# Kernel tuning notes

Hardware: AMD Instinct MI355X
Metric: run time of the kernel (lower is better)

The kernel has to match this reference:

```python
import jax, jax.numpy as jnp
import numpy as np

B, D_IN, NQ, D_OUT = 65536, 1024, 64, 1024
PI = float(np.pi)


def setup_inputs() -> dict:
    key = jax.random.key(0)
    ks = jax.random.split(key, 6)
    return {
        "x": jax.random.normal(ks[0], (B, D_IN), dtype=jnp.float32),
        "W_in": jax.random.normal(ks[1], (NQ, D_IN), dtype=jnp.float32) * 0.02,
        "b_in": jax.random.normal(ks[2], (NQ,), dtype=jnp.float32) * 0.02,
        "quantum_params": jax.random.normal(ks[3], (NQ, 3), dtype=jnp.float32) * 0.1,
        "W_out": jax.random.normal(ks[4], (D_OUT, NQ), dtype=jnp.float32) * 0.02,
        "b_out": jax.random.normal(ks[5], (D_OUT,), dtype=jnp.float32) * 0.02,
    }


def reference(x, W_in, b_in, quantum_params, W_out, b_out):
    # input linear + tanh: [B, NQ]
    h = jnp.tanh(x @ W_in.T + b_in)
    # quantum forward, vectorized over (batch, qubit):
    # state = cos(h*pi/2)*cos(p0) + sin(p1)*cos(p2)
    angles = h * PI
    p0, p1, p2 = quantum_params[:, 0], quantum_params[:, 1], quantum_params[:, 2]
    state = jnp.cos(angles * 0.5) * jnp.cos(p0) + jnp.sin(p1) * jnp.cos(p2)
    # output linear: [B, D_OUT]
    return state @ W_out.T + b_out
```

## Files before the change

kernel.cpp:

```cpp
#include <hip/hip_runtime.h>
#include <hip/hip_bf16.h>
#include <math.h>

#define NB 65536
#define DIN 1024
#define NQ 64
#define DOUT 1024

typedef __attribute__((ext_vector_type(8))) short bf16x8;
typedef __attribute__((ext_vector_type(4))) float f32x4;
typedef unsigned short u16;

__device__ __forceinline__ u16 f2bf(float f) {
    union { float f; unsigned u; } v; v.f = f;
    return (u16)((v.u + 0x7fffu + ((v.u >> 16) & 1u)) >> 16);
}

__device__ __forceinline__ void gll16(const void* g, void* l) {
    __builtin_amdgcn_global_load_lds(
        (const __attribute__((address_space(1))) unsigned int*)g,
        (__attribute__((address_space(3))) unsigned int*)l, 16, 0, 0);
}
__device__ __forceinline__ void gll4(const void* g, void* l) {
    __builtin_amdgcn_global_load_lds(
        (const __attribute__((address_space(1))) unsigned int*)g,
        (__attribute__((address_space(3))) unsigned int*)l, 4, 0, 0);
}

__global__ __launch_bounds__(256) void kP(const float* __restrict__ W_in,
                                          const float* __restrict__ W_out,
                                          const float* __restrict__ qp,
                                          u16* __restrict__ Wbf,
                                          u16* __restrict__ Wobf,
                                          float* __restrict__ cp0,
                                          float* __restrict__ cq) {
    int tid = blockIdx.x * 256 + threadIdx.x;
    {
        int j = tid & 7, l = (tid >> 3) & 63, n = (tid >> 9) & 3, c = tid >> 11;
        int row = n * 16 + (l & 15);
        int k   = c * 32 + (l >> 4) * 8 + j;
        Wbf[tid] = f2bf(W_in[row * DIN + k]);
    }
    {
        int j = tid & 7, l = (tid >> 3) & 63, kf = (tid >> 9) & 1, n = tid >> 10;
        int col = n * 16 + (l & 15);
        int k   = kf * 32 + (l >> 4) * 8 + j;
        Wobf[tid] = f2bf(W_out[col * NQ + k]);
    }
    if (tid < NQ) {
        cp0[tid] = cosf(qp[tid * 3 + 0]);
        cq[tid]  = sinf(qp[tid * 3 + 1]) * cosf(qp[tid * 3 + 2]);
    }
}

__global__ __launch_bounds__(64) void kF(const float* __restrict__ x,
                                         const u16* __restrict__ Wbf,
                                         const float* __restrict__ b_in,
                                         const float* __restrict__ cp0,
                                         const float* __restrict__ cq,
                                         const u16* __restrict__ Wobf,
                                         const float* __restrict__ b_out,
                                         float* __restrict__ out) {
    __shared__ __align__(16) char  ring[3 * 6144];
    __shared__ __align__(16) u16   st[16][72];
    __shared__ __align__(16) float boutL[DOUT];
    __shared__ __align__(16) float binL[NQ], cp0L[NQ], cqL[NQ];

    const int l = threadIdx.x;
    const int r = l & 15, kg = l >> 4;
    const int row0 = blockIdx.x * 16;

    gll4(b_in + l, binL);
    gll4(cp0 + l, cp0L);
    gll4(cq  + l, cqL);
    gll16(b_out + l * 4 +   0, (char*)boutL);
    gll16(b_out + l * 4 + 256, (char*)boutL + 1024);
    gll16(b_out + l * 4 + 512, (char*)boutL + 2048);
    gll16(b_out + l * 4 + 768, (char*)boutL + 3072);

    const char* xs1 = (const char*)x + (size_t)(row0 + (l >> 3)) * (DIN * 4)
                                     + (size_t)((((l & 7) ^ (l >> 3))) * 16);
    const char* xs2 = xs1 + (size_t)8 * DIN * 4;
    const char* wsrc = (const char*)Wbf  + l * 16;
    const char* osrc = (const char*)Wobf + l * 16;

#define STAGE_A(t) { char* buf_ = ring + ((t) % 3) * 6144; \
    gll16(xs1 + (size_t)(t) * 128, buf_); \
    gll16(xs2 + (size_t)(t) * 128, buf_ + 1024); \
    const char* ws_ = wsrc + (size_t)(t) * 4096; \
    gll16(ws_,        buf_ + 2048); \
    gll16(ws_ + 1024, buf_ + 3072); \
    gll16(ws_ + 2048, buf_ + 4096); \
    gll16(ws_ + 3072, buf_ + 5120); }

#define STAGE_B(g) { char* ob_ = ring + ((g) % 3) * 4096; \
    const char* os_ = osrc + (size_t)(g) * 4096; \
    gll16(os_,        ob_); \
    gll16(os_ + 1024, ob_ + 1024); \
    gll16(os_ + 2048, ob_ + 2048); \
    gll16(os_ + 3072, ob_ + 3072); }

    STAGE_A(0) STAGE_A(1)

    f32x4 acc[4] = {f32x4{0,0,0,0}, f32x4{0,0,0,0}, f32x4{0,0,0,0}, f32x4{0,0,0,0}};
    const int sA = (2 * kg) ^ (r & 7);
    const int sB = sA ^ 1;

    #pragma unroll
    for (int t = 0; t < 32; ++t) {
        if (t <= 29) STAGE_A(t + 2)
        if (t <= 29)      asm volatile("s_waitcnt vmcnt(12)" ::: "memory");
        else if (t == 30) asm volatile("s_waitcnt vmcnt(6)"  ::: "memory");
        else              asm volatile("s_waitcnt vmcnt(0)"  ::: "memory");
        const char* buf = ring + (t % 3) * 6144;
        const char* xrow = buf + (r >> 3) * 1024 + (r & 7) * 128;
        float4 xa = *(const float4*)(xrow + sA * 16);
        float4 xb = *(const float4*)(xrow + sB * 16);
        union { bf16x8 v; unsigned u[4]; } a;
        asm("v_cvt_pk_bf16_f32 %0, %1, %2" : "=v"(a.u[0]) : "v"(xa.x), "v"(xa.y));
        asm("v_cvt_pk_bf16_f32 %0, %1, %2" : "=v"(a.u[1]) : "v"(xa.z), "v"(xa.w));
        asm("v_cvt_pk_bf16_f32 %0, %1, %2" : "=v"(a.u[2]) : "v"(xb.x), "v"(xb.y));
        asm("v_cvt_pk_bf16_f32 %0, %1, %2" : "=v"(a.u[3]) : "v"(xb.z), "v"(xb.w));
        #pragma unroll
        for (int n = 0; n < 4; ++n) {
            bf16x8 b = *(const bf16x8*)(buf + 2048 + n * 1024 + l * 16);
            acc[n] = __builtin_amdgcn_mfma_f32_16x16x32_bf16(a.v, b, acc[n], 0, 0, 0);
        }
    }

    STAGE_B(0) STAGE_B(1)

    #pragma unroll
    for (int n = 0; n < 4; ++n) {
        int q = n * 16 + r;
        float bi = binL[q], c0q = cp0L[q], c1q = cqL[q];
        #pragma unroll
        for (int i = 0; i < 4; ++i) {
            float av = acc[n][i] + bi;
            float e2 = __builtin_amdgcn_exp2f(av * 2.8853900817779268f);
            float th = 1.0f - 2.0f * __builtin_amdgcn_rcpf(e2 + 1.0f);
            float sv = __builtin_amdgcn_cosf(th * 0.25f) * c0q + c1q;
            st[kg * 4 + i][q] = f2bf(sv);
        }
    }
    bf16x8 sa0 = *(const bf16x8*)&st[r][kg * 8];
    bf16x8 sa1 = *(const bf16x8*)&st[r][32 + kg * 8];

    const char* outS = (const char*)out + (size_t)row0 * DOUT * 4;
    unsigned vo[4];
    #pragma unroll
    for (int i = 0; i < 4; ++i)
        vo[i] = (unsigned)(kg * 4 + i) * (DOUT * 4) + r * 4;

    #pragma unroll
    for (int g = 0; g < 32; ++g) {
        if (g <= 29) STAGE_B(g + 2)
        if (g == 0)       asm volatile("s_waitcnt vmcnt(8)"  ::: "memory");
        else if (g == 1)  asm volatile("s_waitcnt vmcnt(16)" ::: "memory");
        else if (g <= 29) asm volatile("s_waitcnt vmcnt(24)" ::: "memory");
        else if (g == 30) asm volatile("s_waitcnt vmcnt(20)" ::: "memory");
        else              asm volatile("s_waitcnt vmcnt(16)" ::: "memory");
        const char* ob = ring + (g % 3) * 4096;
        #pragma unroll
        for (int ti = 0; ti < 2; ++ti) {
            const int tile = g * 2 + ti;
            bf16x8 b0 = *(const bf16x8*)(ob + ti * 2048 + l * 16);
            bf16x8 b1 = *(const bf16x8*)(ob + ti * 2048 + 1024 + l * 16);
            f32x4 a2 = {0.0f, 0.0f, 0.0f, 0.0f};
            a2 = __builtin_amdgcn_mfma_f32_16x16x32_bf16(sa0, b0, a2, 0, 0, 0);
            a2 = __builtin_amdgcn_mfma_f32_16x16x32_bf16(sa1, b1, a2, 0, 0, 0);
            float bo = boutL[tile * 16 + r];
            #pragma unroll
            for (int i = 0; i < 4; ++i) {
                float d = a2[i] + bo;
                asm volatile("global_store_dword %0, %1, %2 offset:%3"
                             :: "v"(vo[i]), "v"(d), "s"(outS), "i"(tile * 64) : "memory");
            }
        }
    }
#undef STAGE_A
#undef STAGE_B
}

extern "C" void kernel_launch(void* const* d_in, const int* in_sizes, int n_in,
                              void* d_out, int out_size, void* d_ws, size_t ws_size,
                              hipStream_t stream) {
    const float* x    = (const float*)d_in[0];
    const float* W_in = (const float*)d_in[1];
    const float* b_in = (const float*)d_in[2];
    const float* qp   = (const float*)d_in[3];
    const float* W_out= (const float*)d_in[4];
    const float* b_out= (const float*)d_in[5];
    float* out = (float*)d_out;

    char* ws = (char*)d_ws;
    u16*   Wbf  = (u16*)(ws);
    u16*   Wobf = (u16*)(ws + 131072);
    float* cp0  = (float*)(ws + 262144);
    float* cq   = (float*)(ws + 262400);

    kP<<<256, 256, 0, stream>>>(W_in, W_out, qp, Wbf, Wobf, cp0, cq);
    kF<<<NB / 16, 64, 0, stream>>>(x, Wbf, b_in, cp0, cq, Wobf, b_out, out);
}
```

Measured before the change: 158.1 us.

## Stage x in larger row chunks and stage output through LDS for wide stores

Reorganizes the fused kernel's LDS into one arena. x is now loaded in 512-byte row chunks every four k-steps instead of 128-byte slices each step, and the W_in and W_out rings are split into separate buffers so W_out prefetch can start before the first GEMM ends. Output tiles are staged in LDS and written as coalesced 16-byte row stores rather than scattered dword stores. The aim is to cut global memory transaction overhead on both the input and output streams, at the cost of larger LDS use (44KB per block), which lowers occupancy, and more complex vmcnt bookkeeping.

```diff
diff --git a/kernel.cpp b/kernel.cpp
--- a/kernel.cpp
+++ b/kernel.cpp
@@ -61,74 +61,81 @@
                                          const u16* __restrict__ Wobf,
                                          const float* __restrict__ b_out,
                                          float* __restrict__ out) {
-    __shared__ __align__(16) char  ring[3 * 6144];
-    __shared__ __align__(16) u16   st[16][72];
-    __shared__ __align__(16) float boutL[DOUT];
-    __shared__ __align__(16) float binL[NQ], cp0L[NQ], cqL[NQ];
+    __shared__ __align__(16) char arena[44032];
 
     const int l = threadIdx.x;
     const int r = l & 15, kg = l >> 4;
+    const int r7 = r & 7;
     const int row0 = blockIdx.x * 16;
 
-    gll4(b_in + l, binL);
-    gll4(cp0 + l, cp0L);
-    gll4(cq  + l, cqL);
-    gll16(b_out + l * 4 +   0, (char*)boutL);
-    gll16(b_out + l * 4 + 256, (char*)boutL + 1024);
-    gll16(b_out + l * 4 + 512, (char*)boutL + 2048);
-    gll16(b_out + l * 4 + 768, (char*)boutL + 3072);
-
-    const char* xs1 = (const char*)x + (size_t)(row0 + (l >> 3)) * (DIN * 4)
-                                     + (size_t)((((l & 7) ^ (l >> 3))) * 16);
-    const char* xs2 = xs1 + (size_t)8 * DIN * 4;
-    const char* wsrc = (const char*)Wbf  + l * 16;
-    const char* osrc = (const char*)Wobf + l * 16;
-
-#define STAGE_A(t) { char* buf_ = ring + ((t) % 3) * 6144; \
-    gll16(xs1 + (size_t)(t) * 128, buf_); \
-    gll16(xs2 + (size_t)(t) * 128, buf_ + 1024); \
-    const char* ws_ = wsrc + (size_t)(t) * 4096; \
-    gll16(ws_,        buf_ + 2048); \
-    gll16(ws_ + 1024, buf_ + 3072); \
-    gll16(ws_ + 2048, buf_ + 4096); \
-    gll16(ws_ + 3072, buf_ + 5120); }
-
-#define STAGE_B(g) { char* ob_ = ring + ((g) % 3) * 4096; \
-    const char* os_ = osrc + (size_t)(g) * 4096; \
-    gll16(os_,        ob_); \
-    gll16(os_ + 1024, ob_ + 1024); \
-    gll16(os_ + 2048, ob_ + 2048); \
-    gll16(os_ + 3072, ob_ + 3072); }
-
-    STAGE_A(0) STAGE_A(1)
+    float* binL  = (float*)(arena + 39168);
+    float* cp0L  = (float*)(arena + 39424);
+    float* cqL   = (float*)(arena + 39680);
+    float* boutL = (float*)(arena + 39936);
+    u16 (*st)[72] = (u16(*)[72])(arena + 36864);
+
+    gll4(b_in + l, arena + 39168);
+    gll4(cp0 + l, arena + 39424);
+    gll4(cq  + l, arena + 39680);
+    gll16(b_out + l * 4 +   0, arena + 39936);
+    gll16(b_out + l * 4 + 256, arena + 39936 + 1024);
+    gll16(b_out + l * 4 + 512, arena + 39936 + 2048);
+    gll16(b_out + l * 4 + 768, arena + 39936 + 3072);
+
+    const int h = l >> 5;
+    const int q32 = (l & 31) ^ h;
+    const char* xbase = (const char*)x + (size_t)(row0 + h) * 4096;
+
+#define STAGE_P(p) { char* d_ = arena + ((p) % 3) * 8192; \
+    _Pragma("unroll") \
+    for (int j_ = 0; j_ < 8; ++j_) { \
+        const char* s_ = xbase + (size_t)(2 * j_) * 4096 + (p) * 512 \
+                         + ((q32 ^ ((j_ & 3) << 1)) * 16); \
+        gll16(s_, d_ + j_ * 1024); } }
+
+#define STAGE_W(t) { char* d_ = arena + 24576 + ((t) % 3) * 4096; \
+    const char* s_ = (const char*)Wbf + (size_t)(t) * 4096 + l * 16; \
+    gll16(s_, d_); gll16(s_ + 1024, d_ + 1024); \
+    gll16(s_ + 2048, d_ + 2048); gll16(s_ + 3072, d_ + 3072); }
+
+#define STAGE_G(k) { char* d_ = arena + 16384 + ((k) % 4) * 4096; \
+    const char* s_ = (const char*)Wobf + (size_t)(k) * 4096 + l * 16; \
+    gll16(s_, d_); gll16(s_ + 1024, d_ + 1024); \
+    gll16(s_ + 2048, d_ + 2048); gll16(s_ + 3072, d_ + 3072); }
+
+#define VMW(n) { asm volatile("s_waitcnt vmcnt(" #n ")" ::: "memory"); \
+                 __builtin_amdgcn_sched_barrier(0); }
+
+    STAGE_P(0) STAGE_P(1) STAGE_W(0) STAGE_W(1)
 
     f32x4 acc[4] = {f32x4{0,0,0,0}, f32x4{0,0,0,0}, f32x4{0,0,0,0}, f32x4{0,0,0,0}};
-    const int sA = (2 * kg) ^ (r & 7);
-    const int sB = sA ^ 1;
 
     #pragma unroll
     for (int t = 0; t < 32; ++t) {
-        if (t <= 29) STAGE_A(t + 2)
-        if (t <= 29)      asm volatile("s_waitcnt vmcnt(12)" ::: "memory");
-        else if (t == 30) asm volatile("s_waitcnt vmcnt(6)"  ::: "memory");
-        else              asm volatile("s_waitcnt vmcnt(0)"  ::: "memory");
-        const char* buf = ring + (t % 3) * 6144;
-        const char* xrow = buf + (r >> 3) * 1024 + (r & 7) * 128;
-        float4 xa = *(const float4*)(xrow + sA * 16);
-        float4 xb = *(const float4*)(xrow + sB * 16);
+        if (t + 2 <= 31) STAGE_W(t + 2)
+        if ((t & 3) == 0 && t <= 20) STAGE_P((t >> 2) + 2)
+        if (t == 31) { STAGE_G(0) STAGE_G(1) STAGE_G(2) }
+        const int NA = (t <= 22 && (t & 3) <= 2) ? 16
+                     : (t <= 29 ? 8 : (t == 30 ? 4 : 12));
+        if (NA == 16) VMW(16) else if (NA == 8) VMW(8)
+        else if (NA == 4) VMW(4) else VMW(12)
+
+        const char* xb_ = arena + ((t >> 2) % 3) * 8192 + r * 512;
+        const int s = t & 3;
+        f32x4 xa = *(const f32x4*)(xb_ + (((s * 8 + kg * 2 + 0) ^ r7) * 16));
+        f32x4 xc = *(const f32x4*)(xb_ + (((s * 8 + kg * 2 + 1) ^ r7) * 16));
         union { bf16x8 v; unsigned u[4]; } a;
-        asm("v_cvt_pk_bf16_f32 %0, %1, %2" : "=v"(a.u[0]) : "v"(xa.x), "v"(xa.y));
-        asm("v_cvt_pk_bf16_f32 %0, %1, %2" : "=v"(a.u[1]) : "v"(xa.z), "v"(xa.w));
-        asm("v_cvt_pk_bf16_f32 %0, %1, %2" : "=v"(a.u[2]) : "v"(xb.x), "v"(xb.y));
-        asm("v_cvt_pk_bf16_f32 %0, %1, %2" : "=v"(a.u[3]) : "v"(xb.z), "v"(xb.w));
+        asm("v_cvt_pk_bf16_f32 %0, %1, %2" : "=v"(a.u[0]) : "v"(xa[0]), "v"(xa[1]));
+        asm("v_cvt_pk_bf16_f32 %0, %1, %2" : "=v"(a.u[1]) : "v"(xa[2]), "v"(xa[3]));
+        asm("v_cvt_pk_bf16_f32 %0, %1, %2" : "=v"(a.u[2]) : "v"(xc[0]), "v"(xc[1]));
+        asm("v_cvt_pk_bf16_f32 %0, %1, %2" : "=v"(a.u[3]) : "v"(xc[2]), "v"(xc[3]));
+        const char* wb_ = arena + 24576 + (t % 3) * 4096;
         #pragma unroll
         for (int n = 0; n < 4; ++n) {
-            bf16x8 b = *(const bf16x8*)(buf + 2048 + n * 1024 + l * 16);
+            bf16x8 b = *(const bf16x8*)(wb_ + n * 1024 + l * 16);
             acc[n] = __builtin_amdgcn_mfma_f32_16x16x32_bf16(a.v, b, acc[n], 0, 0, 0);
         }
     }
-
-    STAGE_B(0) STAGE_B(1)
 
     #pragma unroll
     for (int n = 0; n < 4; ++n) {
@@ -146,40 +153,55 @@
     bf16x8 sa0 = *(const bf16x8*)&st[r][kg * 8];
     bf16x8 sa1 = *(const bf16x8*)&st[r][32 + kg * 8];
 
-    const char* outS = (const char*)out + (size_t)row0 * DOUT * 4;
-    unsigned vo[4];
+    float* outst = (float*)arena;
     #pragma unroll
-    for (int i = 0; i < 4; ++i)
-        vo[i] = (unsigned)(kg * 4 + i) * (DOUT * 4) + r * 4;
-
-    #pragma unroll
-    for (int g = 0; g < 32; ++g) {
-        if (g <= 29) STAGE_B(g + 2)
-        if (g == 0)       asm volatile("s_waitcnt vmcnt(8)"  ::: "memory");
-        else if (g == 1)  asm volatile("s_waitcnt vmcnt(16)" ::: "memory");
-        else if (g <= 29) asm volatile("s_waitcnt vmcnt(24)" ::: "memory");
-        else if (g == 30) asm volatile("s_waitcnt vmcnt(20)" ::: "memory");
-        else              asm volatile("s_waitcnt vmcnt(16)" ::: "memory");
-        const char* ob = ring + (g % 3) * 4096;
+    for (int k = 0; k < 32; ++k) {
+        if (k + 3 <= 31) STAGE_G(k + 3)
+        const int NBw = (k >= 8 && (k & 7) <= 2) ? 28
+                      : (k <= 28 ? 12 : (k == 29 ? 8 : (k == 30 ? 4 : 0)));
+        if (NBw == 28) VMW(28) else if (NBw == 12) VMW(12)
+        else if (NBw == 8) VMW(8) else if (NBw == 4) VMW(4) else VMW(0)
+
+        const char* gb = arena + 16384 + (k % 4) * 4096;
         #pragma unroll
         for (int ti = 0; ti < 2; ++ti) {
-            const int tile = g * 2 + ti;
-            bf16x8 b0 = *(const bf16x8*)(ob + ti * 2048 + l * 16);
-            bf16x8 b1 = *(const bf16x8*)(ob + ti * 2048 + 1024 + l * 16);
+            bf16x8 b0 = *(const bf16x8*)(gb + ti * 2048 + l * 16);
+            bf16x8 b1 = *(const bf16x8*)(gb + ti * 2048 + 1024 + l * 16);
             f32x4 a2 = {0.0f, 0.0f, 0.0f, 0.0f};
             a2 = __builtin_amdgcn_mfma_f32_16x16x32_bf16(sa0, b0, a2, 0, 0, 0);
             a2 = __builtin_amdgcn_mfma_f32_16x16x32_bf16(sa1, b1, a2, 0, 0, 0);
+            const int tile = 2 * k + ti;
+            const int c0 = ((tile & 15) << 4) + r;
             float bo = boutL[tile * 16 + r];
             #pragma unroll
-            for (int i = 0; i < 4; ++i) {
-                float d = a2[i] + bo;
-                asm volatile("global_store_dword %0, %1, %2 offset:%3"
-                             :: "v"(vo[i]), "v"(d), "s"(outS), "i"(tile * 64) : "memory");
+            for (int i = 0; i < 4; ++i)
+                outst[(kg * 4 + i) * 256 + c0] = a2[i] + bo;
+        }
+        if ((k & 7) == 7) {
+            const int cb = k >> 3;
+            #pragma unroll
+            for (int j = 0; j < 16; ++j) {
+                f32x4 v = *(const f32x4*)((const char*)outst + j * 1024 + l * 16);
+                const char* oS = (const char*)out + (size_t)(row0 + j) * 4096;
+                if (cb == 0)
+                    asm volatile("global_store_dwordx4 %0, %1, %2 offset:0"
+                                 :: "v"(l * 16), "v"(v), "s"(oS) : "memory");
+                else if (cb == 1)
+                    asm volatile("global_store_dwordx4 %0, %1, %2 offset:1024"
+                                 :: "v"(l * 16), "v"(v), "s"(oS) : "memory");
+                else if (cb == 2)
+                    asm volatile("global_store_dwordx4 %0, %1, %2 offset:2048"
+                                 :: "v"(l * 16), "v"(v), "s"(oS) : "memory");
+                else
+                    asm volatile("global_store_dwordx4 %0, %1, %2 offset:3072"
+                                 :: "v"(l * 16), "v"(v), "s"(oS) : "memory");
             }
         }
     }
-#undef STAGE_A
-#undef STAGE_B
+#undef STAGE_P
+#undef STAGE_W
+#undef STAGE_G
+#undef VMW
 }
 
 extern "C" void kernel_launch(void* const* d_in, const int* in_sizes, int n_in,
```

Measured after the change: 172.5 us. 9.1% more time.
